# Optimization experiments

Measured on AMD Instinct MI355X. Metric: run time of the kernel, lower is better.

The kernel has to match this reference:

```python
import jax, jax.numpy as jnp
import numpy as np

BN_EPS = 1e-5


def conv1x1(x, W, b):
    # x: (B, Cin, H, Wd); W: (Cout, Cin); b: (Cout,)
    return jnp.einsum('bchw,oc->bohw', x, W) + b[None, :, None, None]


def maxpool2x2(x):
    B, C, H, Wd = x.shape
    return x.reshape(B, C, H // 2, 2, Wd // 2, 2).max(axis=(3, 5))


def batchnorm_train(x, gamma, beta):
    # training-mode BN over (B, H, W) per channel, NCHW
    mean = x.mean(axis=(0, 2, 3), keepdims=True)
    var = x.var(axis=(0, 2, 3), keepdims=True)
    xn = (x - mean) * jax.lax.rsqrt(var + BN_EPS)
    return xn * gamma[None, :, None, None] + beta[None, :, None, None]


def setup_inputs() -> dict:
    key = jax.random.key(0)
    ks = jax.random.split(key, 11)
    C, Ci = 256, 128
    scale = 1.0 / np.sqrt(C)
    x = jax.random.normal(ks[0], (4, C, 96, 96), dtype=jnp.float32)
    Wg = jax.random.normal(ks[1], (Ci, C), dtype=jnp.float32) * scale
    bg = jax.random.normal(ks[2], (Ci,), dtype=jnp.float32) * 0.01
    Wt = jax.random.normal(ks[3], (Ci, C), dtype=jnp.float32) * scale
    bt = jax.random.normal(ks[4], (Ci,), dtype=jnp.float32) * 0.01
    Wp = jax.random.normal(ks[5], (Ci, C), dtype=jnp.float32) * scale
    bp = jax.random.normal(ks[6], (Ci,), dtype=jnp.float32) * 0.01
    Ww = jax.random.normal(ks[7], (C, Ci), dtype=jnp.float32) * (1.0 / np.sqrt(Ci))
    bw = jax.random.normal(ks[8], (C,), dtype=jnp.float32) * 0.01
    gamma = jax.random.uniform(ks[9], (C,), dtype=jnp.float32)
    beta = jax.random.normal(ks[10], (C,), dtype=jnp.float32) * 0.01
    return {'x': x, 'Wg': Wg, 'bg': bg, 'Wt': Wt, 'bt': bt, 'Wp': Wp,
            'bp': bp, 'Ww': Ww, 'bw': bw, 'gamma': gamma, 'beta': beta}


def reference(x, Wg, bg, Wt, bt, Wp, bp, Ww, bw, gamma, beta):
    B, C, H, Wd = x.shape
    Ci = Wg.shape[0]
    # g, phi: 1x1 conv then 2x2 maxpool (sub_sample_factor=2)
    g_x = maxpool2x2(conv1x1(x, Wg, bg)).reshape(B, Ci, -1)          # (B, Ci, M)
    phi_x = maxpool2x2(conv1x1(x, Wp, bp)).reshape(B, Ci, -1)        # (B, Ci, M)
    theta_x = conv1x1(x, Wt, bt).reshape(B, Ci, -1)                  # (B, Ci, N)
    # embedded-gaussian attention: softmax(theta^T phi) g^T
    f = jnp.einsum('bcn,bcm->bnm', theta_x, phi_x)                   # (B, N, M)
    a = jax.nn.softmax(f, axis=-1)
    y = jnp.einsum('bnm,bcm->bcn', a, g_x).reshape(B, Ci, H, Wd)
    # W: 1x1 conv + BN (training-mode batch stats), then residual
    W_y = batchnorm_train(conv1x1(y, Ww, bw), gamma, beta)
    return W_y + x
```

## Files before the change

kernel.cpp:

```cpp
#include <hip/hip_runtime.h>
#include <hip/hip_bf16.h>

#define BB 4
#define CC 256
#define CI 128
#define NPIX 9216
#define MPIX 2304
#define WIMG 96
#define WPOOL 48

typedef _Float16 f16x2 __attribute__((ext_vector_type(2)));
typedef _Float16 f16x4 __attribute__((ext_vector_type(4)));
typedef _Float16 f16x8 __attribute__((ext_vector_type(8)));
typedef float f32x4 __attribute__((ext_vector_type(4)));

static __device__ __forceinline__ void gload16(const void* g, void* lds) {
  __builtin_amdgcn_global_load_lds(
      (const __attribute__((address_space(1))) unsigned int*)g,
      (__attribute__((address_space(3))) unsigned int*)lds, 16, 0, 0);
}

__global__ __launch_bounds__(256) void k_prep(
    const float* __restrict__ Wt, const float* __restrict__ Wg,
    const float* __restrict__ Wp, const float* __restrict__ Ww,
    _Float16* __restrict__ Wall, _Float16* __restrict__ Wwh)
{
  int i = blockIdx.x * 256 + threadIdx.x;
  if (i < 98304) {
    int o = i >> 8, c = i & 255;
    float v = (o < 128) ? Wt[o * 256 + c]
            : (o < 256) ? Wg[(o - 128) * 256 + c]
                        : Wp[(o - 256) * 256 + c];
    Wall[i] = (_Float16)v;
  } else {
    int j = i - 98304;
    Wwh[j] = (_Float16)Ww[j];
  }
}

__global__ __launch_bounds__(256) void k_xt(
    const float* __restrict__ x, _Float16* __restrict__ xt)
{
  const int nt = blockIdx.x, ct = blockIdx.y, b = blockIdx.z;
  const int n0 = nt * 64, c0 = ct * 64;
  __shared__ float L[64][65];
  const int t = threadIdx.x;
  #pragma unroll
  for (int i = 0; i < 16; ++i) {
    int idx = i * 256 + t, c = idx >> 6, n = idx & 63;
    L[c][n] = x[(size_t)(b * CC + c0 + c) * NPIX + n0 + n];
  }
  __syncthreads();
  #pragma unroll
  for (int i = 0; i < 4; ++i) {
    int idx = i * 256 + t, n = idx >> 4, cg = idx & 15;
    f16x4 v;
    v[0] = (_Float16)L[cg * 4 + 0][n]; v[1] = (_Float16)L[cg * 4 + 1][n];
    v[2] = (_Float16)L[cg * 4 + 2][n]; v[3] = (_Float16)L[cg * 4 + 3][n];
    *(f16x4*)&xt[(size_t)(b * NPIX + n0 + n) * 256 + c0 + cg * 4] = v;
  }
}

__global__ __launch_bounds__(256) void k_convA(
    const _Float16* __restrict__ xt, const _Float16* __restrict__ Wall,
    const float* __restrict__ bt, const float* __restrict__ bg,
    const float* __restrict__ bp,
    _Float16* __restrict__ th_h, _Float16* __restrict__ gphi)
{
  const int pt = blockIdx.x, ot = blockIdx.y, b = blockIdx.z;
  const int p0 = pt * 128, o0 = ot * 128;
  __shared__ char smem[34816];
  char* WsB = smem;
  char* XsB = smem + 8192;
  const int tid = threadIdx.x;
  const int l = tid & 63, w = tid >> 6;
  const int l15 = l & 15, g16 = l >> 4;
  const int wo = (w & 1) * 64, wp = (w >> 1) * 64;

  f32x4 acc[4][4] = {};
  for (int k0 = 0; k0 < 256; k0 += 32) {
    #pragma unroll
    for (int i = 0; i < 2; ++i) {
      int idx = i * 256 + tid, r = idx >> 2, cg = idx & 3;
      int sw = (cg ^ ((r >> 1) & 3)) * 16;
      *(int4*)(WsB + r * 64 + sw) =
          *(const int4*)&Wall[(size_t)(o0 + r) * 256 + k0 + cg * 8];
      *(int4*)(XsB + r * 64 + sw) =
          *(const int4*)&xt[(size_t)(b * NPIX + p0 + r) * 256 + k0 + cg * 8];
    }
    __syncthreads();
    f16x8 af[4], bf[4];
    #pragma unroll
    for (int f = 0; f < 4; ++f) {
      int ro = wo + f * 16 + l15;
      af[f] = *(const f16x8*)(WsB + ro * 64 + ((g16 ^ ((ro >> 1) & 3)) * 16));
      int rp = wp + f * 16 + l15;
      bf[f] = *(const f16x8*)(XsB + rp * 64 + ((g16 ^ ((rp >> 1) & 3)) * 16));
    }
    #pragma unroll
    for (int of = 0; of < 4; ++of)
      #pragma unroll
      for (int pf = 0; pf < 4; ++pf)
        acc[of][pf] = __builtin_amdgcn_mfma_f32_16x16x32_f16(af[of], bf[pf], acc[of][pf], 0, 0, 0);
    __syncthreads();
  }

  if (o0 == 0) {
    _Float16* T = (_Float16*)smem;
    #pragma unroll
    for (int of = 0; of < 4; ++of) {
      const float4 bb = *(const float4*)&bt[wo + of * 16 + g16 * 4];
      float bv[4] = {bb.x, bb.y, bb.z, bb.w};
      #pragma unroll
      for (int pf = 0; pf < 4; ++pf) {
        f16x4 v;
        #pragma unroll
        for (int r = 0; r < 4; ++r) v[r] = (_Float16)(acc[of][pf][r] + bv[r]);
        *(f16x4*)&T[(wp + pf * 16 + l15) * 136 + wo + of * 16 + g16 * 4] = v;
      }
    }
    __syncthreads();
    #pragma unroll
    for (int i = 0; i < 8; ++i) {
      int idx = i * 256 + tid, row = idx >> 4, cg = idx & 15;
      *(int4*)&th_h[(size_t)(b * NPIX + p0 + row) * 128 + cg * 8] =
          *(const int4*)&T[row * 136 + cg * 8];
    }
  } else {
    const float* bsel = (o0 == 128) ? bg : bp;
    const int chbase = o0 - 128;
    #pragma unroll
    for (int of = 0; of < 4; ++of) {
      const float4 bb = *(const float4*)&bsel[wo + of * 16 + g16 * 4];
      float bv[4] = {bb.x, bb.y, bb.z, bb.w};
      #pragma unroll
      for (int pf = 0; pf < 4; ++pf)
        #pragma unroll
        for (int r = 0; r < 4; ++r) {
          int ch = chbase + wo + of * 16 + g16 * 4 + r;
          gphi[(size_t)(b * 256 + ch) * NPIX + p0 + wp + pf * 16 + l15] =
              (_Float16)(acc[of][pf][r] + bv[r]);
        }
    }
  }
}

__global__ __launch_bounds__(256) void k_pool2(
    const _Float16* __restrict__ gphi,
    _Float16* __restrict__ g_h, _Float16* __restrict__ phi_h)
{
  const int mt = blockIdx.x, ct = blockIdx.y, b = blockIdx.z;
  const int m0 = mt * 64, c0 = ct * 32;
  __shared__ _Float16 Lg[32][72], Lp[32][72];
  const int t = threadIdx.x;
  #pragma unroll
  for (int i = 0; i < 8; ++i) {
    int idx = i * 256 + t, c = idx >> 6, m = idx & 63;
    int mm = m0 + m, hp = mm / WPOOL, wp = mm % WPOOL;
    const _Float16* sg = &gphi[(size_t)(b * 256 + c0 + c) * NPIX + hp * 192 + wp * 2];
    f16x2 a0 = *(const f16x2*)sg;
    f16x2 a1 = *(const f16x2*)(sg + WIMG);
    Lg[c][m] = (_Float16)fmaxf(fmaxf((float)a0[0], (float)a0[1]),
                               fmaxf((float)a1[0], (float)a1[1]));
    const _Float16* sp = sg + (size_t)128 * NPIX;
    f16x2 b0 = *(const f16x2*)sp;
    f16x2 b1 = *(const f16x2*)(sp + WIMG);
    Lp[c][m] = (_Float16)fmaxf(fmaxf((float)b0[0], (float)b0[1]),
                               fmaxf((float)b1[0], (float)b1[1]));
  }
  __syncthreads();
  {
    int c = t >> 3, mq = t & 7;
    f16x8 v = *(const f16x8*)&Lg[c][mq * 8];
    *(f16x8*)&g_h[(size_t)(b * CI + c0 + c) * MPIX + m0 + mq * 8] = v;
  }
  #pragma unroll
  for (int i = 0; i < 2; ++i) {
    int idx = i * 256 + t, m = idx >> 3, cg = idx & 7;
    f16x4 v;
    v[0] = Lp[cg * 4 + 0][m]; v[1] = Lp[cg * 4 + 1][m];
    v[2] = Lp[cg * 4 + 2][m]; v[3] = Lp[cg * 4 + 3][m];
    *(f16x4*)&phi_h[(size_t)(b * MPIX + m0 + m) * 128 + c0 + cg * 4] = v;
  }
}

__global__ __launch_bounds__(256, 2) void k_attn(
    const _Float16* __restrict__ th_h,
    const _Float16* __restrict__ phi_h,
    const _Float16* __restrict__ g_h,
    _Float16* __restrict__ y_part,
    float2* __restrict__ ml)
{
  const int qt = blockIdx.x, b = blockIdx.y, split = blockIdx.z;
  const int n0 = qt * 128;
  const int kt0 = split * 18;
  __shared__ char smem[65536];
  char* const PlB = smem + 49152;

  const int tid = threadIdx.x;
  const int l = tid & 63, wid = tid >> 6;
  const int l15 = l & 15, g16 = l >> 4;
  const int wq0 = wid * 32;

  f16x8 thf[2][4];
  #pragma unroll
  for (int qh = 0; qh < 2; ++qh) {
    const size_t row = (size_t)(b * NPIX + n0 + wq0 + 16 * qh + l15) * 128;
    #pragma unroll
    for (int cs = 0; cs < 4; ++cs)
      thf[qh][cs] = *(const f16x8*)&th_h[row + 32 * cs + 8 * g16];
  }

  auto stage_phi = [&](int bufsel, int kt) {
    char* dst = smem + bufsel * 16384;
    const int m1 = kt * 64;
    #pragma unroll
    for (int j = 0; j < 4; ++j) {
      int mbase = wid * 16 + j * 4;
      int m = mbase + (l >> 4);
      int cg = (l & 15) ^ (m & 7);
      gload16(&phi_h[((size_t)(b * MPIX + m1 + m) << 7) + cg * 8],
              dst + mbase * 256);
    }
  };
  auto stage_g = [&](int kt) {
    char* dst = smem + 32768;
    const int m1 = kt * 64;
    #pragma unroll
    for (int j = 0; j < 4; ++j) {
      int cbase = wid * 32 + j * 8;
      int c = cbase + (l >> 3);
      int cg = (l & 7) ^ (c & 7);
      gload16(&g_h[(size_t)(b * CI + c) * MPIX + m1 + cg * 8],
              dst + cbase * 128);
    }
  };

  stage_phi(0, kt0);
  __syncthreads();

  f32x4 yacc[2][8] = {};
  float mrun[2] = {-1e30f, -1e30f};
  float lrun[2] = {0.f, 0.f};

  #pragma unroll 1
  for (int kt = kt0; kt < kt0 + 18; ++kt) {
    stage_g(kt);
    const char* phC = smem + ((kt - kt0) & 1) * 16384;

    f32x4 sacc[4][2] = {};
    #pragma unroll
    for (int cs = 0; cs < 4; ++cs) {
      const int cb = cs * 64 + g16 * 16;
      #pragma unroll
      for (int mf = 0; mf < 4; ++mf) {
        const int m = 16 * mf + l15;
        f16x8 aph = *(const f16x8*)(phC + m * 256 + (cb ^ ((m & 7) << 4)));
        sacc[mf][0] = __builtin_amdgcn_mfma_f32_16x16x32_f16(aph, thf[0][cs], sacc[mf][0], 0, 0, 0);
        sacc[mf][1] = __builtin_amdgcn_mfma_f32_16x16x32_f16(aph, thf[1][cs], sacc[mf][1], 0, 0, 0);
      }
    }

    float scl2[2];
    f16x4 pr[4][2];
    #pragma unroll
    for (int qh = 0; qh < 2; ++qh) {
      float mx = -1e30f;
      #pragma unroll
      for (int mf = 0; mf < 4; ++mf)
        #pragma unroll
        for (int r = 0; r < 4; ++r) mx = fmaxf(mx, sacc[mf][qh][r]);
      mx = fmaxf(mx, __shfl_xor(mx, 16, 64));
      mx = fmaxf(mx, __shfl_xor(mx, 32, 64));
      const float mo = mrun[qh];
      const float mn = fmaxf(mo, mx);
      float sum = 0.f;
      #pragma unroll
      for (int mf = 0; mf < 4; ++mf)
        #pragma unroll
        for (int r = 0; r < 4; ++r) {
          float p = __expf(sacc[mf][qh][r] - mn);
          _Float16 ph = (_Float16)p;
          pr[mf][qh][r] = ph;
          sum += (float)ph;
        }
      sum += __shfl_xor(sum, 16, 64);
      sum += __shfl_xor(sum, 32, 64);
      const float sc = __expf(mo - mn);
      scl2[qh] = sc;
      lrun[qh] = lrun[qh] * sc + sum;
      mrun[qh] = mn;
    }

    #pragma unroll
    for (int qh = 0; qh < 2; ++qh) {
      const int qw = l15 + 16 * qh;
      char* prow = PlB + (wid << 12) + qw * 128;
      #pragma unroll
      for (int mf = 0; mf < 4; ++mf)
        *(f16x4*)(prow + ((32 * mf + 8 * g16) ^ ((qw & 7) << 4))) = pr[mf][qh];
    }

    {
      float rs[2][4];
      #pragma unroll
      for (int r = 0; r < 4; ++r) {
        rs[0][r] = __shfl(scl2[0], 4 * g16 + r, 64);
        rs[1][r] = __shfl(scl2[1], 4 * g16 + r, 64);
      }
      #pragma unroll
      for (int qi = 0; qi < 2; ++qi)
        #pragma unroll
        for (int cf = 0; cf < 8; ++cf)
          #pragma unroll
          for (int r = 0; r < 4; ++r)
            yacc[qi][cf][r] *= rs[qi][r];
    }

    __syncthreads();

    if (kt + 1 < kt0 + 18)
      stage_phi((kt + 1 - kt0) & 1, kt + 1);

    #pragma unroll
    for (int ms = 0; ms < 2; ++ms) {
      const int mb = ms * 64 + g16 * 16;
      const int q0w = l15, q1w = l15 + 16;
      f16x8 pa0 = *(const f16x8*)(PlB + (wid << 12) + q0w * 128 + (mb ^ ((q0w & 7) << 4)));
      f16x8 pa1 = *(const f16x8*)(PlB + (wid << 12) + q1w * 128 + (mb ^ ((q1w & 7) << 4)));
      #pragma unroll
      for (int cf = 0; cf < 8; ++cf) {
        const int c = 16 * cf + l15;
        f16x8 gb = *(const f16x8*)(smem + 32768 + c * 128 + (mb ^ ((c & 7) << 4)));
        yacc[0][cf] = __builtin_amdgcn_mfma_f32_16x16x32_f16(pa0, gb, yacc[0][cf], 0, 0, 0);
        yacc[1][cf] = __builtin_amdgcn_mfma_f32_16x16x32_f16(pa1, gb, yacc[1][cf], 0, 0, 0);
      }
    }

    __syncthreads();
  }

  if (g16 == 0) {
    #pragma unroll
    for (int qh = 0; qh < 2; ++qh)
      ml[(size_t)(split * BB + b) * NPIX + n0 + wq0 + 16 * qh + l15] =
          make_float2(mrun[qh], lrun[qh]);
  }
  _Float16* Yl = (_Float16*)smem;
  #pragma unroll
  for (int qi = 0; qi < 2; ++qi)
    #pragma unroll
    for (int cf = 0; cf < 8; ++cf)
      #pragma unroll
      for (int r = 0; r < 4; ++r)
        Yl[(wq0 + 16 * qi + 4 * g16 + r) * 136 + 16 * cf + l15] =
            (_Float16)yacc[qi][cf][r];
  __syncthreads();
  #pragma unroll
  for (int i = 0; i < 8; ++i) {
    int idx = i * 256 + tid, row = idx >> 4, cg = idx & 15;
    *(int4*)&y_part[(size_t)((split * BB + b) * NPIX + n0 + row) * 128 + cg * 8] =
        *(const int4*)&Yl[row * 136 + cg * 8];
  }
}

__global__ __launch_bounds__(256) void k_comb(
    const _Float16* __restrict__ y_part, const float2* __restrict__ ml,
    _Float16* __restrict__ y_h)
{
  int idx = blockIdx.x * 256 + threadIdx.x;
  int cg = idx & 15;
  int n  = (idx >> 4) % NPIX;
  int b  = (idx >> 4) / NPIX;
  float2 a0 = ml[(size_t)b * NPIX + n];
  float2 a1 = ml[(size_t)(BB + b) * NPIX + n];
  float M = fmaxf(a0.x, a1.x);
  float w0 = __expf(a0.x - M), w1 = __expf(a1.x - M);
  float inv = 1.0f / (w0 * a0.y + w1 * a1.y);
  w0 *= inv; w1 *= inv;
  f16x8 v0 = *(const f16x8*)&y_part[(size_t)(b * NPIX + n) * 128 + cg * 8];
  f16x8 v1 = *(const f16x8*)&y_part[(size_t)((BB + b) * NPIX + n) * 128 + cg * 8];
  f16x8 o;
  #pragma unroll
  for (int r = 0; r < 8; ++r)
    o[r] = (_Float16)(w0 * (float)v0[r] + w1 * (float)v1[r]);
  *(f16x8*)&y_h[(size_t)(b * NPIX + n) * 128 + cg * 8] = o;
}

__global__ __launch_bounds__(256) void k_wconv(
    const _Float16* __restrict__ y_h, const _Float16* __restrict__ Wwh,
    const float* __restrict__ bw, float* __restrict__ zbuf)
{
  const int nt = blockIdx.x, ot = blockIdx.y, b = blockIdx.z;
  const int n0 = nt * 128, o0 = ot * 128;
  __shared__ char smem[16384];
  char* WsB = smem;
  char* YsB = smem + 8192;
  const int tid = threadIdx.x;
  const int l = tid & 63, w = tid >> 6;
  const int l15 = l & 15, g16 = l >> 4;
  const int wo = (w & 1) * 64, wn = (w >> 1) * 64;

  f32x4 acc[4][4] = {};
  for (int k0 = 0; k0 < 128; k0 += 32) {
    #pragma unroll
    for (int i = 0; i < 2; ++i) {
      int idx = i * 256 + tid, r = idx >> 2, cg = idx & 3;
      int sw = (cg ^ ((r >> 1) & 3)) * 16;
      *(int4*)(WsB + r * 64 + sw) =
          *(const int4*)&Wwh[(size_t)(o0 + r) * 128 + k0 + cg * 8];
      *(int4*)(YsB + r * 64 + sw) =
          *(const int4*)&y_h[(size_t)(b * NPIX + n0 + r) * 128 + k0 + cg * 8];
    }
    __syncthreads();
    f16x8 af[4], bf[4];
    #pragma unroll
    for (int f = 0; f < 4; ++f) {
      int ro = wo + f * 16 + l15;
      af[f] = *(const f16x8*)(WsB + ro * 64 + ((g16 ^ ((ro >> 1) & 3)) * 16));
      int rn = wn + f * 16 + l15;
      bf[f] = *(const f16x8*)(YsB + rn * 64 + ((g16 ^ ((rn >> 1) & 3)) * 16));
    }
    #pragma unroll
    for (int of = 0; of < 4; ++of)
      #pragma unroll
      for (int pf = 0; pf < 4; ++pf)
        acc[of][pf] = __builtin_amdgcn_mfma_f32_16x16x32_f16(af[of], bf[pf], acc[of][pf], 0, 0, 0);
    __syncthreads();
  }
  #pragma unroll
  for (int of = 0; of < 4; ++of) {
    const float4 bb = *(const float4*)&bw[o0 + wo + of * 16 + g16 * 4];
    float bv[4] = {bb.x, bb.y, bb.z, bb.w};
    #pragma unroll
    for (int pf = 0; pf < 4; ++pf)
      #pragma unroll
      for (int r = 0; r < 4; ++r)
        zbuf[(size_t)(b * CC + o0 + wo + of * 16 + g16 * 4 + r) * NPIX +
             n0 + wn + pf * 16 + l15] = acc[of][pf][r] + bv[r];
  }
}

__global__ __launch_bounds__(256) void k_stats(
    const float* __restrict__ zbuf, float* __restrict__ stats)
{
  const int o = blockIdx.x, t = threadIdx.x;
  float s = 0.f, s2 = 0.f;
  for (int b = 0; b < BB; ++b) {
    const float* z = &zbuf[(size_t)(b * CC + o) * NPIX];
    for (int i = t; i < NPIX / 4; i += 256) {
      float4 v = *(const float4*)&z[i * 4];
      s  += v.x + v.y + v.z + v.w;
      s2 += v.x * v.x + v.y * v.y + v.z * v.z + v.w * v.w;
    }
  }
  #pragma unroll
  for (int off = 1; off < 64; off <<= 1) {
    s  += __shfl_xor(s,  off, 64);
    s2 += __shfl_xor(s2, off, 64);
  }
  __shared__ float ls[4], ls2[4];
  if ((t & 63) == 0) { ls[t >> 6] = s; ls2[t >> 6] = s2; }
  __syncthreads();
  if (t == 0) {
    float S  = ls[0] + ls[1] + ls[2] + ls[3];
    float S2 = ls2[0] + ls2[1] + ls2[2] + ls2[3];
    const float invn = 1.0f / (float)(BB * NPIX);
    float mean = S * invn;
    float var  = S2 * invn - mean * mean;
    stats[o] = mean;
    stats[CC + o] = rsqrtf(var + 1e-5f);
  }
}

__global__ __launch_bounds__(256) void k_out(
    const float* __restrict__ zbuf, const float* __restrict__ x,
    const float* __restrict__ gamma, const float* __restrict__ beta,
    const float* __restrict__ stats, float* __restrict__ out)
{
  int idx = blockIdx.x * 256 + threadIdx.x;
  const int total4 = BB * CC * NPIX / 4;
  if (idx >= total4) return;
  size_t e = (size_t)idx * 4;
  int p = (int)(e % NPIX);
  int o = (int)((e / NPIX) % CC);
  int b = (int)(e / ((size_t)CC * NPIX));
  float a  = stats[CC + o] * gamma[o];
  float c0 = beta[o] - stats[o] * a;
  float4 z  = *(const float4*)&zbuf[(size_t)(b * CC + o) * NPIX + p];
  float4 xv = *(const float4*)&x[e];
  float4 rv;
  rv.x = z.x * a + c0 + xv.x;
  rv.y = z.y * a + c0 + xv.y;
  rv.z = z.z * a + c0 + xv.z;
  rv.w = z.w * a + c0 + xv.w;
  *(float4*)&out[e] = rv;
}

extern "C" void kernel_launch(void* const* d_in, const int* in_sizes, int n_in,
                              void* d_out, int out_size, void* d_ws, size_t ws_size,
                              hipStream_t stream)
{
  const float* x     = (const float*)d_in[0];
  const float* Wg    = (const float*)d_in[1];
  const float* bg    = (const float*)d_in[2];
  const float* Wt    = (const float*)d_in[3];
  const float* bt    = (const float*)d_in[4];
  const float* Wp    = (const float*)d_in[5];
  const float* bp    = (const float*)d_in[6];
  const float* Ww    = (const float*)d_in[7];
  const float* bw    = (const float*)d_in[8];
  const float* gamma = (const float*)d_in[9];
  const float* beta  = (const float*)d_in[10];
  float* out = (float*)d_out;

  char* wsb = (char*)d_ws;
  float*    zbuf   = (float*)wsb;
  _Float16* xt     = (_Float16*)wsb;
  _Float16* y_part = (_Float16*)wsb;
  char* p2 = wsb + 37748736;
  _Float16* gphi  = (_Float16*)p2;
  _Float16* y_h   = (_Float16*)p2;
  char* p3 = p2 + 18874368;
  _Float16* th_h  = (_Float16*)p3;
  _Float16* g_h   = (_Float16*)(p3 + 9437184);
  _Float16* phi_h = (_Float16*)(p3 + 11796480);
  _Float16* Wall  = (_Float16*)(p3 + 14155776);
  _Float16* Wwh   = (_Float16*)(p3 + 14352384);
  float*    stats = (float*)(p3 + 14417920);
  float2*   ml    = (float2*)(p3 + 14420992);

  k_prep<<<512, 256, 0, stream>>>(Wt, Wg, Wp, Ww, Wall, Wwh);

  dim3 gxt(NPIX / 64, CC / 64, BB);
  k_xt<<<gxt, 256, 0, stream>>>(x, xt);

  dim3 g1(NPIX / 128, 3, BB);
  k_convA<<<g1, 256, 0, stream>>>(xt, Wall, bt, bg, bp, th_h, gphi);

  dim3 g2(MPIX / 64, 4, BB);
  k_pool2<<<g2, 256, 0, stream>>>(gphi, g_h, phi_h);

  dim3 g3(NPIX / 128, BB, 2);
  k_attn<<<g3, 256, 0, stream>>>(th_h, phi_h, g_h, y_part, ml);

  k_comb<<<(BB * NPIX * 16) / 256, 256, 0, stream>>>(y_part, ml, y_h);

  dim3 g4(NPIX / 128, CC / 128, BB);
  k_wconv<<<g4, 256, 0, stream>>>(y_h, Wwh, bw, zbuf);

  k_stats<<<CC, 256, 0, stream>>>(zbuf, stats);

  k_out<<<(BB * CC * NPIX / 4 + 255) / 256, 256, 0, stream>>>(zbuf, x, gamma, beta, stats, out);
}
```

Baseline: 174.7 us.

## Store W-conv output as fp16, fold log2e into theta, raise MFMA priority

Theta is pre-scaled by log2(e) in the conv epilogue so the softmax can use exp2f instead of __expf, and the combine kernel is changed to match. s_setprio is raised around the two MFMA loops in the attention kernel. The W-conv output buffer is also changed from fp32 to fp16, which halves the traffic of writing it and reading it back in the stats and output kernels. The cost is reduced precision in the BN input and in its batch statistics.

```diff
diff --git a/kernel.cpp b/kernel.cpp
--- a/kernel.cpp
+++ b/kernel.cpp
@@ -8,6 +8,7 @@
 #define MPIX 2304
 #define WIMG 96
 #define WPOOL 48
+#define LOG2E 1.4426950408889634f
 
 typedef _Float16 f16x2 __attribute__((ext_vector_type(2)));
 typedef _Float16 f16x4 __attribute__((ext_vector_type(4)));
@@ -115,7 +116,8 @@
       for (int pf = 0; pf < 4; ++pf) {
         f16x4 v;
         #pragma unroll
-        for (int r = 0; r < 4; ++r) v[r] = (_Float16)(acc[of][pf][r] + bv[r]);
+        for (int r = 0; r < 4; ++r)
+          v[r] = (_Float16)((acc[of][pf][r] + bv[r]) * LOG2E);
         *(f16x4*)&T[(wp + pf * 16 + l15) * 136 + wo + of * 16 + g16 * 4] = v;
       }
     }
@@ -195,6 +197,7 @@
   const int n0 = qt * 128;
   const int kt0 = split * 18;
   __shared__ char smem[65536];
+  char* const GlB = smem + 32768;
   char* const PlB = smem + 49152;
 
   const int tid = threadIdx.x;
@@ -224,7 +227,6 @@
     }
   };
   auto stage_g = [&](int kt) {
-    char* dst = smem + 32768;
     const int m1 = kt * 64;
     #pragma unroll
     for (int j = 0; j < 4; ++j) {
@@ -232,7 +234,7 @@
       int c = cbase + (l >> 3);
       int cg = (l & 7) ^ (c & 7);
       gload16(&g_h[(size_t)(b * CI + c) * MPIX + m1 + cg * 8],
-              dst + cbase * 128);
+              GlB + cbase * 128);
     }
   };
 
@@ -249,6 +251,7 @@
     const char* phC = smem + ((kt - kt0) & 1) * 16384;
 
     f32x4 sacc[4][2] = {};
+    __builtin_amdgcn_s_setprio(1);
     #pragma unroll
     for (int cs = 0; cs < 4; ++cs) {
       const int cb = cs * 64 + g16 * 16;
@@ -260,6 +263,7 @@
         sacc[mf][1] = __builtin_amdgcn_mfma_f32_16x16x32_f16(aph, thf[1][cs], sacc[mf][1], 0, 0, 0);
       }
     }
+    __builtin_amdgcn_s_setprio(0);
 
     float scl2[2];
     f16x4 pr[4][2];
@@ -279,14 +283,14 @@
       for (int mf = 0; mf < 4; ++mf)
         #pragma unroll
         for (int r = 0; r < 4; ++r) {
-          float p = __expf(sacc[mf][qh][r] - mn);
+          float p = exp2f(sacc[mf][qh][r] - mn);
           _Float16 ph = (_Float16)p;
           pr[mf][qh][r] = ph;
           sum += (float)ph;
         }
       sum += __shfl_xor(sum, 16, 64);
       sum += __shfl_xor(sum, 32, 64);
-      const float sc = __expf(mo - mn);
+      const float sc = exp2f(mo - mn);
       scl2[qh] = sc;
       lrun[qh] = lrun[qh] * sc + sum;
       mrun[qh] = mn;
@@ -322,6 +326,7 @@
     if (kt + 1 < kt0 + 18)
       stage_phi((kt + 1 - kt0) & 1, kt + 1);
 
+    __builtin_amdgcn_s_setprio(1);
     #pragma unroll
     for (int ms = 0; ms < 2; ++ms) {
       const int mb = ms * 64 + g16 * 16;
@@ -331,11 +336,12 @@
       #pragma unroll
       for (int cf = 0; cf < 8; ++cf) {
         const int c = 16 * cf + l15;
-        f16x8 gb = *(const f16x8*)(smem + 32768 + c * 128 + (mb ^ ((c & 7) << 4)));
+        f16x8 gb = *(const f16x8*)(GlB + c * 128 + (mb ^ ((c & 7) << 4)));
         yacc[0][cf] = __builtin_amdgcn_mfma_f32_16x16x32_f16(pa0, gb, yacc[0][cf], 0, 0, 0);
         yacc[1][cf] = __builtin_amdgcn_mfma_f32_16x16x32_f16(pa1, gb, yacc[1][cf], 0, 0, 0);
       }
     }
+    __builtin_amdgcn_s_setprio(0);
 
     __syncthreads();
   }
@@ -375,7 +381,7 @@
   float2 a0 = ml[(size_t)b * NPIX + n];
   float2 a1 = ml[(size_t)(BB + b) * NPIX + n];
   float M = fmaxf(a0.x, a1.x);
-  float w0 = __expf(a0.x - M), w1 = __expf(a1.x - M);
+  float w0 = exp2f(a0.x - M), w1 = exp2f(a1.x - M);
   float inv = 1.0f / (w0 * a0.y + w1 * a1.y);
   w0 *= inv; w1 *= inv;
   f16x8 v0 = *(const f16x8*)&y_part[(size_t)(b * NPIX + n) * 128 + cg * 8];
@@ -389,7 +395,7 @@
 
 __global__ __launch_bounds__(256) void k_wconv(
     const _Float16* __restrict__ y_h, const _Float16* __restrict__ Wwh,
-    const float* __restrict__ bw, float* __restrict__ zbuf)
+    const float* __restrict__ bw, _Float16* __restrict__ z_h)
 {
   const int nt = blockIdx.x, ot = blockIdx.y, b = blockIdx.z;
   const int n0 = nt * 128, o0 = ot * 128;
@@ -436,22 +442,25 @@
     for (int pf = 0; pf < 4; ++pf)
       #pragma unroll
       for (int r = 0; r < 4; ++r)
-        zbuf[(size_t)(b * CC + o0 + wo + of * 16 + g16 * 4 + r) * NPIX +
-             n0 + wn + pf * 16 + l15] = acc[of][pf][r] + bv[r];
+        z_h[(size_t)(b * CC + o0 + wo + of * 16 + g16 * 4 + r) * NPIX +
+            n0 + wn + pf * 16 + l15] = (_Float16)(acc[of][pf][r] + bv[r]);
   }
 }
 
 __global__ __launch_bounds__(256) void k_stats(
-    const float* __restrict__ zbuf, float* __restrict__ stats)
+    const _Float16* __restrict__ z_h, float* __restrict__ stats)
 {
   const int o = blockIdx.x, t = threadIdx.x;
   float s = 0.f, s2 = 0.f;
   for (int b = 0; b < BB; ++b) {
-    const float* z = &zbuf[(size_t)(b * CC + o) * NPIX];
-    for (int i = t; i < NPIX / 4; i += 256) {
-      float4 v = *(const float4*)&z[i * 4];
-      s  += v.x + v.y + v.z + v.w;
-      s2 += v.x * v.x + v.y * v.y + v.z * v.z + v.w * v.w;
+    const _Float16* z = &z_h[(size_t)(b * CC + o) * NPIX];
+    for (int i = t; i < NPIX / 8; i += 256) {
+      f16x8 v = *(const f16x8*)&z[i * 8];
+      #pragma unroll
+      for (int r = 0; r < 8; ++r) {
+        float f = (float)v[r];
+        s += f; s2 += f * f;
+      }
     }
   }
   #pragma unroll
@@ -474,27 +483,33 @@
 }
 
 __global__ __launch_bounds__(256) void k_out(
-    const float* __restrict__ zbuf, const float* __restrict__ x,
+    const _Float16* __restrict__ z_h, const float* __restrict__ x,
     const float* __restrict__ gamma, const float* __restrict__ beta,
     const float* __restrict__ stats, float* __restrict__ out)
 {
   int idx = blockIdx.x * 256 + threadIdx.x;
-  const int total4 = BB * CC * NPIX / 4;
-  if (idx >= total4) return;
-  size_t e = (size_t)idx * 4;
+  const int total8 = BB * CC * NPIX / 8;
+  if (idx >= total8) return;
+  size_t e = (size_t)idx * 8;
   int p = (int)(e % NPIX);
   int o = (int)((e / NPIX) % CC);
   int b = (int)(e / ((size_t)CC * NPIX));
   float a  = stats[CC + o] * gamma[o];
   float c0 = beta[o] - stats[o] * a;
-  float4 z  = *(const float4*)&zbuf[(size_t)(b * CC + o) * NPIX + p];
-  float4 xv = *(const float4*)&x[e];
-  float4 rv;
-  rv.x = z.x * a + c0 + xv.x;
-  rv.y = z.y * a + c0 + xv.y;
-  rv.z = z.z * a + c0 + xv.z;
-  rv.w = z.w * a + c0 + xv.w;
-  *(float4*)&out[e] = rv;
+  f16x8 z = *(const f16x8*)&z_h[(size_t)(b * CC + o) * NPIX + p];
+  float4 x0 = *(const float4*)&x[e];
+  float4 x1 = *(const float4*)&x[e + 4];
+  float4 r0, r1;
+  r0.x = (float)z[0] * a + c0 + x0.x;
+  r0.y = (float)z[1] * a + c0 + x0.y;
+  r0.z = (float)z[2] * a + c0 + x0.z;
+  r0.w = (float)z[3] * a + c0 + x0.w;
+  r1.x = (float)z[4] * a + c0 + x1.x;
+  r1.y = (float)z[5] * a + c0 + x1.y;
+  r1.z = (float)z[6] * a + c0 + x1.z;
+  r1.w = (float)z[7] * a + c0 + x1.w;
+  *(float4*)&out[e] = r0;
+  *(float4*)&out[e + 4] = r1;
 }
 
 extern "C" void kernel_launch(void* const* d_in, const int* in_sizes, int n_in,
@@ -515,9 +530,9 @@
   float* out = (float*)d_out;
 
   char* wsb = (char*)d_ws;
-  float*    zbuf   = (float*)wsb;
   _Float16* xt     = (_Float16*)wsb;
   _Float16* y_part = (_Float16*)wsb;
+  _Float16* z_h    = (_Float16*)wsb;
   char* p2 = wsb + 37748736;
   _Float16* gphi  = (_Float16*)p2;
   _Float16* y_h   = (_Float16*)p2;
@@ -547,9 +562,9 @@
   k_comb<<<(BB * NPIX * 16) / 256, 256, 0, stream>>>(y_part, ml, y_h);
 
   dim3 g4(NPIX / 128, CC / 128, BB);
-  k_wconv<<<g4, 256, 0, stream>>>(y_h, Wwh, bw, zbuf);
-
-  k_stats<<<CC, 256, 0, stream>>>(zbuf, stats);
-
-  k_out<<<(BB * CC * NPIX / 4 + 255) / 256, 256, 0, stream>>>(zbuf, x, gamma, beta, stats, out);
-}
+  k_wconv<<<g4, 256, 0, stream>>>(y_h, Wwh, bw, z_h);
+
+  k_stats<<<CC, 256, 0, stream>>>(z_h, stats);
+
+  k_out<<<(BB * CC * NPIX / 8 + 255) / 256, 256, 0, stream>>>(z_h, x, gamma, beta, stats, out);
+}
```

Measured after the change: 183.8 us. +5.2%, slower.
